# Performance work log

Measured on AMD Instinct MI355X. Metric: run time of the kernel, lower is better.

Reference implementation:

```python
import jax, jax.numpy as jnp
import numpy as np

D_MODEL = 1024
NUM_HEADS = 16
DEPTH = D_MODEL // NUM_HEADS


def setup_inputs() -> dict:
    key = jax.random.key(0)
    ks = jax.random.split(key, 9)
    s = 1.0 / np.sqrt(D_MODEL)
    x = jax.random.normal(ks[0], (2, 2048, D_MODEL), dtype=jnp.float32)
    def lin(kw, kb):
        W = jax.random.uniform(kw, (D_MODEL, D_MODEL), jnp.float32, -s, s)
        b = jax.random.uniform(kb, (D_MODEL,), jnp.float32, -s, s)
        return W, b
    Wq, bq = lin(ks[1], ks[2])
    Wk, bk = lin(ks[3], ks[4])
    Wv, bv = lin(ks[5], ks[6])
    Wo, bo = lin(ks[7], ks[8])
    return {"x": x, "Wq": Wq, "bq": bq, "Wk": Wk, "bk": bk,
            "Wv": Wv, "bv": bv, "Wo": Wo, "bo": bo}


def reference(x, Wq, bq, Wk, bk, Wv, bv, Wo, bo):
    B, T, _ = x.shape
    # projections; weights stored as [in, out] (torch Linear applies x @ W.T; here W is already [in,out])
    def split_heads(y):
        return y.reshape(B, T, NUM_HEADS, DEPTH).transpose(0, 2, 1, 3)  # [B,H,T,D]
    Q = split_heads(x @ Wq + bq)
    K = split_heads(x @ Wk + bk)
    V = split_heads(x @ Wv + bv)
    scale = 1.0 / jnp.sqrt(jnp.asarray(DEPTH, dtype=x.dtype))
    scores = jnp.einsum('bhqd,bhkd->bhqk', Q, K) * scale  # [B,H,T,T]
    attn = jax.nn.softmax(scores, axis=-1)
    out = jnp.einsum('bhqk,bhkd->bhqd', attn, V)  # [B,H,T,D]
    out = out.transpose(0, 2, 1, 3).reshape(B, T, D_MODEL)
    return out @ Wo + bo
```

## Files before the change

kernel.cpp:

```cpp
#include <hip/hip_runtime.h>
#include <hip/hip_bf16.h>

typedef unsigned short ushort_t;
typedef short s8v __attribute__((ext_vector_type(8)));
typedef float f4v __attribute__((ext_vector_type(4)));
typedef float f16v __attribute__((ext_vector_type(16)));

#define DM 1024
#define TT 2048
#define NH 16
#define DH 64
#define QSCALE 0.18033688011112042f

__device__ __forceinline__ ushort_t f2bf(float f) {
  union { float f; unsigned u; } v; v.f = f;
  unsigned u = v.u;
  return (ushort_t)((u + 0x7fffu + ((u >> 16) & 1u)) >> 16);
}

__device__ __forceinline__ float bf2f(ushort_t s) {
  union { unsigned u; float f; } v;
  v.u = ((unsigned)s) << 16;
  return v.f;
}

__device__ __forceinline__ unsigned pk2bf(float a, float b) {
  union { __hip_bfloat162 h; unsigned u; } v;
  v.h = __float22bfloat162_rn(float2{a, b});
  return v.u;
}

__device__ __forceinline__ f16v splat16(float x) {
  f16v v;
#pragma unroll
  for (int i = 0; i < 16; i++) v[i] = x;
  return v;
}

__device__ __forceinline__ void gll16(const void* g, const void* l) {
  __builtin_amdgcn_global_load_lds(
      (const __attribute__((address_space(1))) unsigned int*)g,
      (__attribute__((address_space(3))) unsigned int*)l, 16, 0, 0);
}

__global__ __launch_bounds__(256) void prep_kernel(const float* __restrict__ W0,
                                                   const float* __restrict__ W1,
                                                   const float* __restrict__ W2,
                                                   const float* __restrict__ W3,
                                                   const float* __restrict__ x,
                                                   ushort_t* __restrict__ dst,
                                                   ushort_t* __restrict__ xb) {
  __shared__ float tile[32][33];
  const int z = blockIdx.z;
  if (z == 4) {
    int lb = blockIdx.y * 32 + blockIdx.x;
    int i = lb * 256 + threadIdx.x;
    const float4* p = (const float4*)x + (size_t)i * 4;
    float4 a = p[0], b = p[1], c = p[2], d = p[3];
    union { ushort_t s[16]; uint4 u[2]; } r;
    r.s[0] = f2bf(a.x); r.s[1] = f2bf(a.y); r.s[2] = f2bf(a.z); r.s[3] = f2bf(a.w);
    r.s[4] = f2bf(b.x); r.s[5] = f2bf(b.y); r.s[6] = f2bf(b.z); r.s[7] = f2bf(b.w);
    r.s[8] = f2bf(c.x); r.s[9] = f2bf(c.y); r.s[10] = f2bf(c.z); r.s[11] = f2bf(c.w);
    r.s[12] = f2bf(d.x); r.s[13] = f2bf(d.y); r.s[14] = f2bf(d.z); r.s[15] = f2bf(d.w);
    ((uint4*)xb)[(size_t)i * 2] = r.u[0];
    ((uint4*)xb)[(size_t)i * 2 + 1] = r.u[1];
    return;
  }
  const float* W = z == 0 ? W0 : (z == 1 ? W1 : (z == 2 ? W2 : W3));
  ushort_t* Wt = dst + (size_t)z * DM * DM;
  int tx = threadIdx.x & 31, ty = threadIdx.x >> 5;
  int n0 = blockIdx.x * 32, k0 = blockIdx.y * 32;
#pragma unroll
  for (int i = 0; i < 4; i++)
    tile[ty + i * 8][tx] = W[(size_t)(k0 + ty + i * 8) * DM + n0 + tx];
  __syncthreads();
#pragma unroll
  for (int i = 0; i < 4; i++)
    Wt[(size_t)(n0 + ty + i * 8) * DM + k0 + tx] = f2bf(tile[tx][ty + i * 8]);
}

__global__ __launch_bounds__(256) void vtrans_kernel(const ushort_t* __restrict__ V,
                                                     ushort_t* __restrict__ Vt) {
  __shared__ ushort_t Ls[64][72];
  const int t = threadIdx.x;
  const int t0 = blockIdx.x * 64, bh = blockIdx.y;
  const ushort_t* Vb = V + (size_t)bh * TT * DH;
  ushort_t* Vtb = Vt + (size_t)bh * DH * TT;
#pragma unroll
  for (int c = t; c < 512; c += 256) {
    int tt = c & 63, dch = c >> 6;
    union { uint4 u; ushort_t s[8]; } uu;
    uu.u = *(const uint4*)&Vb[(size_t)(t0 + tt) * DH + dch * 8];
#pragma unroll
    for (int i = 0; i < 8; i++) Ls[dch * 8 + i][tt] = uu.s[i];
  }
  __syncthreads();
#pragma unroll
  for (int c = t; c < 512; c += 256) {
    int d = c >> 3, tch = c & 7;
    uint4 u = *(const uint4*)&Ls[d][tch * 8];
    *(uint4*)&Vtb[(size_t)d * TT + t0 + tch * 8] = u;
  }
}

template <int MT, int MODE>
__global__ __launch_bounds__(256) void gemm_bt(
    const ushort_t* __restrict__ A, const ushort_t* __restrict__ Bt,
    const float* __restrict__ bias0, const float* __restrict__ bias1,
    const float* __restrict__ bias2,
    ushort_t* __restrict__ qo, ushort_t* __restrict__ ko, ushort_t* __restrict__ vo,
    float* __restrict__ co) {
  constexpr int TM = MT * 32;
  __shared__ __align__(16) ushort_t Asm[2][TM * 32];
  __shared__ __align__(16) ushort_t Bsm[2][128 * 32];
  const int m0 = blockIdx.x * TM, n0 = blockIdx.y * 128;
  const int t = threadIdx.x, lane = t & 63;
  const int wid = t >> 6, wr = wid >> 1, wc = wid & 1;
  const ushort_t* Ab = A + (size_t)m0 * DM;
  const ushort_t* Bb = Bt + (size_t)n0 * DM;

  f4v zero = {0.f, 0.f, 0.f, 0.f};
  f4v acc[MT][4];
#pragma unroll
  for (int i = 0; i < MT; i++)
#pragma unroll
    for (int j = 0; j < 4; j++) acc[i][j] = zero;

  const int r0 = t >> 2;
  const int csw = ((t & 3) ^ ((r0 >> 1) & 3)) * 8;
  const int rr = lane & 15, q8 = lane >> 4;

#define GSTAGE(kb, bb)                                                   \
  do {                                                                   \
    int k0_ = (kb) * 32 + csw;                                           \
    gll16(Ab + (size_t)r0 * DM + k0_, &Asm[bb][t * 8]);                  \
    if constexpr (MT == 4)                                               \
      gll16(Ab + (size_t)(r0 + 64) * DM + k0_, &Asm[bb][(t + 256) * 8]); \
    gll16(Bb + (size_t)r0 * DM + k0_, &Bsm[bb][t * 8]);                  \
    gll16(Bb + (size_t)(r0 + 64) * DM + k0_, &Bsm[bb][(t + 256) * 8]);   \
  } while (0)

  GSTAGE(0, 0);
  for (int kb = 0; kb < 32; ++kb) {
    const int cur = kb & 1;
    if (kb < 31) {
      GSTAGE(kb + 1, cur ^ 1);
      if constexpr (MT == 4)
        asm volatile("s_waitcnt vmcnt(4)" ::: "memory");
      else
        asm volatile("s_waitcnt vmcnt(3)" ::: "memory");
    } else {
      asm volatile("s_waitcnt vmcnt(0)" ::: "memory");
    }
    __builtin_amdgcn_s_barrier();
    __builtin_amdgcn_sched_barrier(0);

    s8v af[MT], bf_[4];
#pragma unroll
    for (int mt = 0; mt < MT; mt++) {
      int row = wr * (MT * 16) + mt * 16 + rr;
      af[mt] = *(const s8v*)&Asm[cur][row * 32 + ((q8 ^ ((row >> 1) & 3)) << 3)];
    }
#pragma unroll
    for (int nt = 0; nt < 4; nt++) {
      int row = wc * 64 + nt * 16 + rr;
      bf_[nt] = *(const s8v*)&Bsm[cur][row * 32 + ((q8 ^ ((row >> 1) & 3)) << 3)];
    }
    __builtin_amdgcn_s_setprio(1);
#pragma unroll
    for (int mt = 0; mt < MT; mt++)
#pragma unroll
      for (int nt = 0; nt < 4; nt++)
        acc[mt][nt] =
            __builtin_amdgcn_mfma_f32_16x16x32_bf16(af[mt], bf_[nt], acc[mt][nt], 0, 0, 0);
    __builtin_amdgcn_s_setprio(0);
    __builtin_amdgcn_sched_barrier(0);
    __builtin_amdgcn_s_barrier();
  }
#undef GSTAGE

  const int col_l = lane & 15, row_q = (lane >> 4) * 4;
  if (MODE == 0) {
    const int qkv = n0 >> 10;
    const float* bias = qkv == 0 ? bias0 : (qkv == 1 ? bias1 : bias2);
    ushort_t* dst = qkv == 0 ? qo : (qkv == 1 ? ko : vo);
    const float sc = qkv == 0 ? QSCALE : 1.0f;
    const int nb = n0 & 1023;
#pragma unroll
    for (int nt = 0; nt < 4; nt++) {
      int gc = nb + wc * 64 + nt * 16 + col_l;
      float bv_ = bias[gc];
      int hh = gc >> 6, d = gc & 63;
#pragma unroll
      for (int mt = 0; mt < MT; mt++) {
#pragma unroll
        for (int j = 0; j < 4; j++) {
          int r = m0 + wr * (MT * 16) + mt * 16 + row_q + j;
          int bb = r >> 11, tt_ = r & 2047;
          dst[(((size_t)(bb * NH + hh)) * TT + tt_) * DH + d] = f2bf((acc[mt][nt][j] + bv_) * sc);
        }
      }
    }
  } else {
#pragma unroll
    for (int nt = 0; nt < 4; nt++) {
      int gc = n0 + wc * 64 + nt * 16 + col_l;
      float bv_ = bias0[gc];
#pragma unroll
      for (int mt = 0; mt < MT; mt++) {
#pragma unroll
        for (int j = 0; j < 4; j++) {
          int r = m0 + wr * (MT * 16) + mt * 16 + row_q + j;
          co[(size_t)r * DM + gc] = acc[mt][nt][j] + bv_;
        }
      }
    }
  }
}

__global__ __launch_bounds__(256, 4) void attn_kernel(const ushort_t* __restrict__ Q,
                                                      const ushort_t* __restrict__ K,
                                                      const ushort_t* __restrict__ Vt,
                                                      ushort_t* __restrict__ Opart,
                                                      float2* __restrict__ stats, int ntiles) {
  __shared__ __align__(16) ushort_t Ksm[2][64 * 64];
  __shared__ __align__(16) ushort_t Vsm[2][64 * 64];

  const int b_lin = blockIdx.x + (blockIdx.y << 4);
  const int xcd = b_lin & 7, n = b_lin >> 3;
  const int bh = (xcd << 2) | (n >> 4);
  const int qt = n & 15;
  const int z = blockIdx.z;
  const int b = bh >> 4, h = bh & 15;
  const int t = threadIdx.x, lane = t & 63, wid = t >> 6;
  const int lo = lane & 31, hi = lane >> 5;
  const ushort_t* Qb = Q + ((size_t)bh * TT + qt * 128 + wid * 32) * DH;
  const ushort_t* Kb = K + (size_t)bh * TT * DH;
  const ushort_t* Vb = Vt + (size_t)bh * DH * TT;
  ushort_t* Op = Opart + (size_t)z * (2 * TT) * DM;

  s8v qf[4];
#pragma unroll
  for (int ks = 0; ks < 4; ks++)
    qf[ks] = *(const s8v*)&Qb[lo * 64 + ks * 16 + hi * 8];

  f16v oacc[2];
  oacc[0] = splat16(0.f);
  oacc[1] = splat16(0.f);
  float mreg = 0.f, lreg = 0.f;

  const int c0r = t >> 3, c0s = ((t & 7) ^ (c0r & 7)) * 8;
  const int c1 = t + 256;
  const int c1r = c1 >> 3, c1s = ((t & 7) ^ (c1r & 7)) * 8;
  const int tv0 = z * ntiles;

#define STAGE(tv, bb)                                              \
  do {                                                             \
    int kv0_ = (tv) * 64;                                          \
    gll16(&Kb[(size_t)(kv0_ + c0r) * DH + c0s], &Ksm[bb][t * 8]);  \
    gll16(&Vb[(size_t)c0r * TT + kv0_ + c0s], &Vsm[bb][t * 8]);    \
    gll16(&Kb[(size_t)(kv0_ + c1r) * DH + c1s], &Ksm[bb][c1 * 8]); \
    gll16(&Vb[(size_t)c1r * TT + kv0_ + c1s], &Vsm[bb][c1 * 8]);   \
  } while (0)

  STAGE(tv0, 0);
  for (int it = 0; it < ntiles; ++it) {
    const int cur = it & 1;
    if (it < ntiles - 1) {
      STAGE(tv0 + it + 1, cur ^ 1);
      asm volatile("s_waitcnt vmcnt(4)" ::: "memory");
    } else {
      asm volatile("s_waitcnt vmcnt(0)" ::: "memory");
    }
    __builtin_amdgcn_s_barrier();
    __builtin_amdgcn_sched_barrier(0);

    f16v st0 = splat16(-mreg), st1 = splat16(-mreg);
    __builtin_amdgcn_s_setprio(1);
#pragma unroll
    for (int ks = 0; ks < 4; ks++) {
      int ch = ((ks * 2 + hi) ^ (lo & 7)) << 3;
      s8v kf0 = *(const s8v*)&Ksm[cur][lo * 64 + ch];
      s8v kf1 = *(const s8v*)&Ksm[cur][(32 + lo) * 64 + ch];
      st0 = __builtin_amdgcn_mfma_f32_32x32x16_bf16(kf0, qf[ks], st0, 0, 0, 0);
      st1 = __builtin_amdgcn_mfma_f32_32x32x16_bf16(kf1, qf[ks], st1, 0, 0, 0);
    }
    __builtin_amdgcn_s_setprio(0);

    float pmax = -1e30f;
#pragma unroll
    for (int i = 0; i < 16; i++) pmax = fmaxf(pmax, fmaxf(st0[i], st1[i]));
    pmax = fmaxf(pmax, __shfl_xor(pmax, 32, 64));
    if (!__all(pmax <= 8.0f)) {
      float delta = fmaxf(pmax, 0.f);
      float corr = __builtin_amdgcn_exp2f(-delta);
      mreg += delta;
      st0 -= delta;
      st1 -= delta;
      lreg *= corr;
      oacc[0] *= corr;
      oacc[1] *= corr;
    }
#pragma unroll
    for (int i = 0; i < 16; i++) {
      st0[i] = __builtin_amdgcn_exp2f(st0[i]);
      st1[i] = __builtin_amdgcn_exp2f(st1[i]);
    }
    float ps = 0.f;
#pragma unroll
    for (int i = 0; i < 16; i++) ps += st0[i] + st1[i];
    ps += __shfl_xor(ps, 32, 64);
    lreg += ps;

    s8v pb[4];
#pragma unroll
    for (int kt = 0; kt < 2; kt++) {
#pragma unroll
      for (int s = 0; s < 2; s++) {
        unsigned w0, w1, w2, w3;
        if (kt == 0) {
          w0 = pk2bf(st0[8 * s + 0], st0[8 * s + 1]);
          w1 = pk2bf(st0[8 * s + 2], st0[8 * s + 3]);
          w2 = pk2bf(st0[8 * s + 4], st0[8 * s + 5]);
          w3 = pk2bf(st0[8 * s + 6], st0[8 * s + 7]);
        } else {
          w0 = pk2bf(st1[8 * s + 0], st1[8 * s + 1]);
          w1 = pk2bf(st1[8 * s + 2], st1[8 * s + 3]);
          w2 = pk2bf(st1[8 * s + 4], st1[8 * s + 5]);
          w3 = pk2bf(st1[8 * s + 6], st1[8 * s + 7]);
        }
        asm volatile("v_permlane32_swap_b32 %0, %1" : "+v"(w0), "+v"(w2));
        asm volatile("v_permlane32_swap_b32 %0, %1" : "+v"(w1), "+v"(w3));
        union { unsigned u[4]; s8v v; } pw;
        pw.u[0] = w0; pw.u[1] = w1; pw.u[2] = w2; pw.u[3] = w3;
        pb[kt * 2 + s] = pw.v;
      }
    }

    __builtin_amdgcn_s_setprio(1);
#pragma unroll
    for (int ks = 0; ks < 4; ks++) {
      int ch = ((ks * 2 + hi) ^ (lo & 7)) << 3;
      s8v vf0 = *(const s8v*)&Vsm[cur][lo * 64 + ch];
      s8v vf1 = *(const s8v*)&Vsm[cur][(32 + lo) * 64 + ch];
      oacc[0] = __builtin_amdgcn_mfma_f32_32x32x16_bf16(vf0, pb[ks], oacc[0], 0, 0, 0);
      oacc[1] = __builtin_amdgcn_mfma_f32_32x32x16_bf16(vf1, pb[ks], oacc[1], 0, 0, 0);
    }
    __builtin_amdgcn_s_setprio(0);

    __builtin_amdgcn_sched_barrier(0);
    __builtin_amdgcn_s_barrier();
  }
#undef STAGE

  if (hi == 0) {
    int qrow = qt * 128 + wid * 32 + lo;
    stats[((size_t)(z * 32 + bh)) * TT + qrow] = float2{mreg, lreg};
  }

  ushort_t* Osm = &Ksm[0][0] + wid * 2048;
#pragma unroll
  for (int dt = 0; dt < 2; dt++) {
#pragma unroll
    for (int r = 0; r < 8; r++) {
      int dbase = ((2 * r) & 3) + 8 * ((2 * r) >> 2);
      int d = dt * 32 + dbase + 4 * hi;
      unsigned w = pk2bf(oacc[dt][2 * r], oacc[dt][2 * r + 1]);
      *(unsigned*)&Osm[lo * 64 + (d ^ ((lo & 7) << 3))] = w;
    }
  }
#pragma unroll
  for (int r = 0; r < 4; r++) {
    int q = lane >> 1;
    int chunk = (lane & 1) + r * 2;
    s8v v = *(const s8v*)&Osm[q * 64 + ((chunk ^ (q & 7)) << 3)];
    *(s8v*)&Op[((size_t)(b * TT + qt * 128 + wid * 32 + q)) * DM + h * 64 + chunk * 8] = v;
  }
}

__global__ __launch_bounds__(256) void combine_kernel(const ushort_t* __restrict__ Opart,
                                                      const float2* __restrict__ stats,
                                                      ushort_t* __restrict__ O, int nsplit) {
  int i = blockIdx.x * 256 + threadIdx.x;
  int bt = i >> 7, c = i & 127;
  int b = bt >> 11, t = bt & 2047;
  int bh = b * NH + (c >> 3);
  float2 s0 = stats[(size_t)bh * TT + t];
  union { uint4 u; ushort_t s[8]; } p0, p1, r;
  p0.u = *((const uint4*)Opart + i);
  if (nsplit == 2) {
    float2 s1 = stats[(size_t)(32 + bh) * TT + t];
    p1.u = *((const uint4*)(Opart + (size_t)(2 * TT) * DM) + i);
    float ms = fmaxf(s0.x, s1.x);
    float w0 = __builtin_amdgcn_exp2f(s0.x - ms);
    float w1 = __builtin_amdgcn_exp2f(s1.x - ms);
    float inv = 1.0f / (w0 * s0.y + w1 * s1.y);
#pragma unroll
    for (int j = 0; j < 8; j++)
      r.s[j] = f2bf((w0 * bf2f(p0.s[j]) + w1 * bf2f(p1.s[j])) * inv);
  } else {
    float inv = 1.0f / s0.y;
#pragma unroll
    for (int j = 0; j < 8; j++) r.s[j] = f2bf(bf2f(p0.s[j]) * inv);
  }
  *((uint4*)O + i) = r.u;
}

extern "C" void kernel_launch(void* const* d_in, const int* in_sizes, int n_in,
                              void* d_out, int out_size, void* d_ws, size_t ws_size,
                              hipStream_t stream) {
  const float* x = (const float*)d_in[0];
  const float* Wq = (const float*)d_in[1];
  const float* bq = (const float*)d_in[2];
  const float* Wk = (const float*)d_in[3];
  const float* bk = (const float*)d_in[4];
  const float* Wv = (const float*)d_in[5];
  const float* bv = (const float*)d_in[6];
  const float* Wo = (const float*)d_in[7];
  const float* bo = (const float*)d_in[8];
  float* out = (float*)d_out;

  char* ws = (char*)d_ws;
  ushort_t* xb = (ushort_t*)(ws);
  ushort_t* wqkv = (ushort_t*)(ws + (8ull << 20));
  ushort_t* wot = (ushort_t*)(ws + (14ull << 20));
  ushort_t* Qb = (ushort_t*)(ws + (16ull << 20));
  ushort_t* Kb = (ushort_t*)(ws + (24ull << 20));
  ushort_t* Vb = (ushort_t*)(ws + (32ull << 20));
  ushort_t* Vtb = xb;
  ushort_t* Opart = Vb;
  ushort_t* Ob = Qb;

  const int nsplit = (ws_size >= (49ull << 20)) ? 2 : 1;
  float2* stats = (float2*)(ws + ((nsplit == 2 ? 48ull : 40ull) << 20));

  dim3 tb(256);
  prep_kernel<<<dim3(32, 32, 5), tb, 0, stream>>>(Wq, Wk, Wv, Wo, x, wqkv, xb);
  gemm_bt<4, 0><<<dim3(32, 24), tb, 0, stream>>>(xb, wqkv, bq, bk, bv, Qb, Kb, Vb, nullptr);
  vtrans_kernel<<<dim3(32, 32), tb, 0, stream>>>(Vb, Vtb);
  attn_kernel<<<dim3(16, 32, nsplit), tb, 0, stream>>>(Qb, Kb, Vtb, Opart, stats, 32 / nsplit);
  combine_kernel<<<dim3(2048), tb, 0, stream>>>(Opart, stats, Ob, nsplit);
  gemm_bt<2, 1><<<dim3(64, 8), tb, 0, stream>>>(Ob, wot, bo, nullptr, nullptr, nullptr, nullptr,
                                                nullptr, out);
}
```

Measured before the change: 208.4 us.

## Enlarge QKV GEMM tile to 256x128 with 512 threads and XCD-aware block mapping

The templated GEMM is split into two kernels. The QKV projection now uses 512-thread blocks with a 256x128 output tile (8 waves), halving the grid, and remaps block indices so that blocks on the same XCD share N tiles for L2 reuse. The output projection remaps blocks so each XCD owns one N column of the weight matrix. This trades occupancy and a smaller grid (384 blocks) for more operand reuse per block and better cache locality.

```diff
diff --git a/kernel.cpp b/kernel.cpp
--- a/kernel.cpp
+++ b/kernel.cpp
@@ -103,26 +103,27 @@
   }
 }
 
-template <int MT, int MODE>
-__global__ __launch_bounds__(256) void gemm_bt(
+__global__ __launch_bounds__(512) void gemm_qkv(
     const ushort_t* __restrict__ A, const ushort_t* __restrict__ Bt,
     const float* __restrict__ bias0, const float* __restrict__ bias1,
     const float* __restrict__ bias2,
-    ushort_t* __restrict__ qo, ushort_t* __restrict__ ko, ushort_t* __restrict__ vo,
-    float* __restrict__ co) {
-  constexpr int TM = MT * 32;
-  __shared__ __align__(16) ushort_t Asm[2][TM * 32];
+    ushort_t* __restrict__ qo, ushort_t* __restrict__ ko, ushort_t* __restrict__ vo) {
+  __shared__ __align__(16) ushort_t Asm[2][256 * 32];
   __shared__ __align__(16) ushort_t Bsm[2][128 * 32];
-  const int m0 = blockIdx.x * TM, n0 = blockIdx.y * 128;
+  const int lin = blockIdx.x + blockIdx.y * 16;
+  const int xcd = lin & 7, idx = lin >> 3;
+  const int n_tile = xcd * 3 + (idx % 3);
+  const int m_tile = idx / 3;
+  const int m0 = m_tile * 256, n0 = n_tile * 128;
   const int t = threadIdx.x, lane = t & 63;
   const int wid = t >> 6, wr = wid >> 1, wc = wid & 1;
   const ushort_t* Ab = A + (size_t)m0 * DM;
   const ushort_t* Bb = Bt + (size_t)n0 * DM;
 
   f4v zero = {0.f, 0.f, 0.f, 0.f};
-  f4v acc[MT][4];
-#pragma unroll
-  for (int i = 0; i < MT; i++)
+  f4v acc[4][4];
+#pragma unroll
+  for (int i = 0; i < 4; i++)
 #pragma unroll
     for (int j = 0; j < 4; j++) acc[i][j] = zero;
 
@@ -130,14 +131,12 @@
   const int csw = ((t & 3) ^ ((r0 >> 1) & 3)) * 8;
   const int rr = lane & 15, q8 = lane >> 4;
 
-#define GSTAGE(kb, bb)                                                   \
-  do {                                                                   \
-    int k0_ = (kb) * 32 + csw;                                           \
-    gll16(Ab + (size_t)r0 * DM + k0_, &Asm[bb][t * 8]);                  \
-    if constexpr (MT == 4)                                               \
-      gll16(Ab + (size_t)(r0 + 64) * DM + k0_, &Asm[bb][(t + 256) * 8]); \
-    gll16(Bb + (size_t)r0 * DM + k0_, &Bsm[bb][t * 8]);                  \
-    gll16(Bb + (size_t)(r0 + 64) * DM + k0_, &Bsm[bb][(t + 256) * 8]);   \
+#define GSTAGE(kb, bb)                                                  \
+  do {                                                                  \
+    int k0_ = (kb) * 32 + csw;                                          \
+    gll16(Ab + (size_t)r0 * DM + k0_, &Asm[bb][t * 8]);                 \
+    gll16(Ab + (size_t)(r0 + 128) * DM + k0_, &Asm[bb][(t + 512) * 8]); \
+    gll16(Bb + (size_t)r0 * DM + k0_, &Bsm[bb][t * 8]);                 \
   } while (0)
 
   GSTAGE(0, 0);
@@ -145,20 +144,17 @@
     const int cur = kb & 1;
     if (kb < 31) {
       GSTAGE(kb + 1, cur ^ 1);
-      if constexpr (MT == 4)
-        asm volatile("s_waitcnt vmcnt(4)" ::: "memory");
-      else
-        asm volatile("s_waitcnt vmcnt(3)" ::: "memory");
+      asm volatile("s_waitcnt vmcnt(3)" ::: "memory");
     } else {
       asm volatile("s_waitcnt vmcnt(0)" ::: "memory");
     }
     __builtin_amdgcn_s_barrier();
     __builtin_amdgcn_sched_barrier(0);
 
-    s8v af[MT], bf_[4];
-#pragma unroll
-    for (int mt = 0; mt < MT; mt++) {
-      int row = wr * (MT * 16) + mt * 16 + rr;
+    s8v af[4], bf_[4];
+#pragma unroll
+    for (int mt = 0; mt < 4; mt++) {
+      int row = wr * 64 + mt * 16 + rr;
       af[mt] = *(const s8v*)&Asm[cur][row * 32 + ((q8 ^ ((row >> 1) & 3)) << 3)];
     }
 #pragma unroll
@@ -168,7 +164,7 @@
     }
     __builtin_amdgcn_s_setprio(1);
 #pragma unroll
-    for (int mt = 0; mt < MT; mt++)
+    for (int mt = 0; mt < 4; mt++)
 #pragma unroll
       for (int nt = 0; nt < 4; nt++)
         acc[mt][nt] =
@@ -180,39 +176,107 @@
 #undef GSTAGE
 
   const int col_l = lane & 15, row_q = (lane >> 4) * 4;
-  if (MODE == 0) {
-    const int qkv = n0 >> 10;
-    const float* bias = qkv == 0 ? bias0 : (qkv == 1 ? bias1 : bias2);
-    ushort_t* dst = qkv == 0 ? qo : (qkv == 1 ? ko : vo);
-    const float sc = qkv == 0 ? QSCALE : 1.0f;
-    const int nb = n0 & 1023;
+  const int qkv = n0 >> 10;
+  const float* bias = qkv == 0 ? bias0 : (qkv == 1 ? bias1 : bias2);
+  ushort_t* dst = qkv == 0 ? qo : (qkv == 1 ? ko : vo);
+  const float sc = qkv == 0 ? QSCALE : 1.0f;
+  const int nb = n0 & 1023;
+#pragma unroll
+  for (int nt = 0; nt < 4; nt++) {
+    int gc = nb + wc * 64 + nt * 16 + col_l;
+    float bv_ = bias[gc];
+    int hh = gc >> 6, d = gc & 63;
+#pragma unroll
+    for (int mt = 0; mt < 4; mt++) {
+#pragma unroll
+      for (int j = 0; j < 4; j++) {
+        int r = m0 + wr * 64 + mt * 16 + row_q + j;
+        int bb = r >> 11, tt_ = r & 2047;
+        dst[(((size_t)(bb * NH + hh)) * TT + tt_) * DH + d] = f2bf((acc[mt][nt][j] + bv_) * sc);
+      }
+    }
+  }
+}
+
+__global__ __launch_bounds__(256) void gemm_out(
+    const ushort_t* __restrict__ A, const ushort_t* __restrict__ Bt,
+    const float* __restrict__ bias0, float* __restrict__ co) {
+  __shared__ __align__(16) ushort_t Asm[2][64 * 32];
+  __shared__ __align__(16) ushort_t Bsm[2][128 * 32];
+  const int lin = blockIdx.x + blockIdx.y * 64;
+  const int xcd = lin & 7, idx = lin >> 3;
+  const int m0 = idx * 64, n0 = xcd * 128;
+  const int t = threadIdx.x, lane = t & 63;
+  const int wid = t >> 6, wr = wid >> 1, wc = wid & 1;
+  const ushort_t* Ab = A + (size_t)m0 * DM;
+  const ushort_t* Bb = Bt + (size_t)n0 * DM;
+
+  f4v zero = {0.f, 0.f, 0.f, 0.f};
+  f4v acc[2][4];
+#pragma unroll
+  for (int i = 0; i < 2; i++)
+#pragma unroll
+    for (int j = 0; j < 4; j++) acc[i][j] = zero;
+
+  const int r0 = t >> 2;
+  const int csw = ((t & 3) ^ ((r0 >> 1) & 3)) * 8;
+  const int rr = lane & 15, q8 = lane >> 4;
+
+#define GSTAGE(kb, bb)                                                 \
+  do {                                                                 \
+    int k0_ = (kb) * 32 + csw;                                         \
+    gll16(Ab + (size_t)r0 * DM + k0_, &Asm[bb][t * 8]);                \
+    gll16(Bb + (size_t)r0 * DM + k0_, &Bsm[bb][t * 8]);                \
+    gll16(Bb + (size_t)(r0 + 64) * DM + k0_, &Bsm[bb][(t + 256) * 8]); \
+  } while (0)
+
+  GSTAGE(0, 0);
+  for (int kb = 0; kb < 32; ++kb) {
+    const int cur = kb & 1;
+    if (kb < 31) {
+      GSTAGE(kb + 1, cur ^ 1);
+      asm volatile("s_waitcnt vmcnt(3)" ::: "memory");
+    } else {
+      asm volatile("s_waitcnt vmcnt(0)" ::: "memory");
+    }
+    __builtin_amdgcn_s_barrier();
+    __builtin_amdgcn_sched_barrier(0);
+
+    s8v af[2], bf_[4];
+#pragma unroll
+    for (int mt = 0; mt < 2; mt++) {
+      int row = wr * 32 + mt * 16 + rr;
+      af[mt] = *(const s8v*)&Asm[cur][row * 32 + ((q8 ^ ((row >> 1) & 3)) << 3)];
+    }
 #pragma unroll
     for (int nt = 0; nt < 4; nt++) {
-      int gc = nb + wc * 64 + nt * 16 + col_l;
-      float bv_ = bias[gc];
-      int hh = gc >> 6, d = gc & 63;
-#pragma unroll
-      for (int mt = 0; mt < MT; mt++) {
-#pragma unroll
-        for (int j = 0; j < 4; j++) {
-          int r = m0 + wr * (MT * 16) + mt * 16 + row_q + j;
-          int bb = r >> 11, tt_ = r & 2047;
-          dst[(((size_t)(bb * NH + hh)) * TT + tt_) * DH + d] = f2bf((acc[mt][nt][j] + bv_) * sc);
-        }
-      }
-    }
-  } else {
-#pragma unroll
-    for (int nt = 0; nt < 4; nt++) {
-      int gc = n0 + wc * 64 + nt * 16 + col_l;
-      float bv_ = bias0[gc];
-#pragma unroll
-      for (int mt = 0; mt < MT; mt++) {
-#pragma unroll
-        for (int j = 0; j < 4; j++) {
-          int r = m0 + wr * (MT * 16) + mt * 16 + row_q + j;
-          co[(size_t)r * DM + gc] = acc[mt][nt][j] + bv_;
-        }
+      int row = wc * 64 + nt * 16 + rr;
+      bf_[nt] = *(const s8v*)&Bsm[cur][row * 32 + ((q8 ^ ((row >> 1) & 3)) << 3)];
+    }
+    __builtin_amdgcn_s_setprio(1);
+#pragma unroll
+    for (int mt = 0; mt < 2; mt++)
+#pragma unroll
+      for (int nt = 0; nt < 4; nt++)
+        acc[mt][nt] =
+            __builtin_amdgcn_mfma_f32_16x16x32_bf16(af[mt], bf_[nt], acc[mt][nt], 0, 0, 0);
+    __builtin_amdgcn_s_setprio(0);
+    __builtin_amdgcn_sched_barrier(0);
+    __builtin_amdgcn_s_barrier();
+  }
+#undef GSTAGE
+
+  const int col_l = lane & 15, row_q = (lane >> 4) * 4;
+#pragma unroll
+  for (int nt = 0; nt < 4; nt++) {
+    int gc = n0 + wc * 64 + nt * 16 + col_l;
+    float bv_ = bias0[gc];
+#pragma unroll
+    for (int mt = 0; mt < 2; mt++) {
+#pragma unroll
+      for (int j = 0; j < 4; j++) {
+        int r = m0 + wr * 32 + mt * 16 + row_q + j;
+        co[(size_t)r * DM + gc] = acc[mt][nt][j] + bv_;
       }
     }
   }
@@ -436,10 +500,9 @@
 
   dim3 tb(256);
   prep_kernel<<<dim3(32, 32, 5), tb, 0, stream>>>(Wq, Wk, Wv, Wo, x, wqkv, xb);
-  gemm_bt<4, 0><<<dim3(32, 24), tb, 0, stream>>>(xb, wqkv, bq, bk, bv, Qb, Kb, Vb, nullptr);
+  gemm_qkv<<<dim3(16, 24), dim3(512), 0, stream>>>(xb, wqkv, bq, bk, bv, Qb, Kb, Vb);
   vtrans_kernel<<<dim3(32, 32), tb, 0, stream>>>(Vb, Vtb);
   attn_kernel<<<dim3(16, 32, nsplit), tb, 0, stream>>>(Qb, Kb, Vtb, Opart, stats, 32 / nsplit);
   combine_kernel<<<dim3(2048), tb, 0, stream>>>(Opart, stats, Ob, nsplit);
-  gemm_bt<2, 1><<<dim3(64, 8), tb, 0, stream>>>(Ob, wot, bo, nullptr, nullptr, nullptr, nullptr,
-                                                nullptr, out);
-}
+  gemm_out<<<dim3(64, 8), tb, 0, stream>>>(Ob, wot, bo, out);
+}
```

New measurement: 211.0 us. About the same (+1.2%).
